# Kernel tuning notes

Measured on AMD Instinct MI355X. Metric: run time of the kernel, lower is better.

Reference implementation:

```python
import jax, jax.numpy as jnp
import numpy as np

NUM_LABELS = 1000
HIDDEN = 512
BATCH = 65536
NOISE_STD = 0.1
L_STAB, L_CENTER, L_SEP, L_BRIER = 1.0, 0.1, 0.01, 1.0


def setup_inputs() -> dict:
    key = jax.random.key(0)
    k1, k2, k3, k4, k5 = jax.random.split(key, 5)
    cls_rep = jax.random.normal(k1, (BATCH, HIDDEN), dtype=jnp.float32)
    logits = jax.random.normal(k2, (BATCH, NUM_LABELS), dtype=jnp.float32)
    labels = jax.random.randint(k3, (BATCH,), 0, NUM_LABELS)
    W = jax.random.normal(k4, (HIDDEN, NUM_LABELS), dtype=jnp.float32) * 0.02
    b = jnp.zeros((NUM_LABELS,), dtype=jnp.float32)
    noise = jax.random.normal(k5, (BATCH, HIDDEN), dtype=jnp.float32)
    centers = jnp.zeros((NUM_LABELS, HIDDEN), dtype=jnp.float32)
    return {"cls_rep": cls_rep, "logits": logits, "labels": labels,
            "W": W, "b": b, "noise": noise, "centers": centers}


def _compute_all(cls_rep, logits, labels, W, b, noise, centers):
    # --- update_centers (init branch, no_grad): per-class mean via segment_sum ---
    ones = jnp.ones((cls_rep.shape[0],), dtype=cls_rep.dtype)
    counts = jax.ops.segment_sum(ones, labels, num_segments=NUM_LABELS)           # [C]
    sums = jax.ops.segment_sum(cls_rep, labels, num_segments=NUM_LABELS)          # [C, H]
    present = counts > 0
    batch_means = sums / jnp.maximum(counts, 1.0)[:, None]
    new_centers = jnp.where(present[:, None], batch_means, centers)               # [C, H]
    new_centers = jax.lax.stop_gradient(new_centers)

    # --- stability: classifier(cls_rep + noise_std * eps) vs clean logits ---
    logits_noisy = (cls_rep + NOISE_STD * noise) @ W + b                          # [B, C]
    stab = jnp.mean((logits_noisy - logits) ** 2)

    # --- center loss: gather centroids, MSE ---
    center = jnp.mean((cls_rep - new_centers[labels]) ** 2)

    # --- separation: cdist + exp, minus exp(0)*num_labels ---
    sq = jnp.sum(new_centers ** 2, axis=1)                                        # [C]
    d2 = jnp.maximum(sq[:, None] + sq[None, :] - 2.0 * new_centers @ new_centers.T, 0.0)
    dist = jnp.sqrt(d2)                                                           # [C, C]
    I = jnp.eye(NUM_LABELS, dtype=dist.dtype)
    sep = jnp.sum(jnp.exp(-dist + I)) - jnp.float32(NUM_LABELS)

    # --- brier: softmax vs one-hot ---
    probs = jax.nn.softmax(logits, axis=-1)
    one_hot = jax.nn.one_hot(labels, NUM_LABELS, dtype=logits.dtype)
    brier = jnp.mean(jnp.sum((probs - one_hot) ** 2, axis=1))

    total = L_STAB * stab + L_CENTER * center + L_SEP * sep + L_BRIER * brier
    return jnp.stack([total, stab, center, sep, brier])


def reference(cls_rep, logits, labels, W, b, noise, centers):
    return _compute_all(cls_rep, logits, labels, W, b, noise, centers)
```

## Files before the change

kernel.cpp:

```cpp
#include <hip/hip_runtime.h>

#define BATCH 65536
#define HID   512
#define NCLS  1000
#define NCLSP 1024

typedef long i64;
typedef float f32x4 __attribute__((ext_vector_type(4)));
typedef unsigned short u16;
typedef unsigned int u32;
typedef unsigned char u8;

__device__ __forceinline__ u16 f2bf(float f) {
  u32 u = __float_as_uint(f);
  u += 0x7fffu + ((u >> 16) & 1u);
  return (u16)(u >> 16);
}

__device__ __forceinline__ u32 pk4(float a, float b, float c, float d) {
  u32 r = 0;
  r = (u32)__builtin_amdgcn_cvt_pk_fp8_f32(a, b, (int)r, false);
  r = (u32)__builtin_amdgcn_cvt_pk_fp8_f32(c, d, (int)r, true);
  return r;
}

#define WS_END 2899968
#define WS_BIG 36454400

__global__ void k_hist(const int* __restrict__ labels, int* __restrict__ counts) {
  const int i = blockIdx.x * blockDim.x + threadIdx.x;
  if (i < BATCH) atomicAdd(counts + labels[i], 1);
}

__global__ void k_scan(const int* __restrict__ counts, int* __restrict__ offsets) {
  __shared__ int tmp[1024];
  const int t = threadIdx.x;
  const int v = counts[t];
  tmp[t] = v;
  __syncthreads();
  for (int d = 1; d < 1024; d <<= 1) {
    int u = (t >= d) ? tmp[t - d] : 0;
    __syncthreads();
    tmp[t] += u;
    __syncthreads();
  }
  offsets[t] = tmp[t] - v;
}

__global__ void k_scatter(const int* __restrict__ labels, int* __restrict__ offsets,
                          int* __restrict__ order) {
  const int i = blockIdx.x * blockDim.x + threadIdx.x;
  if (i < BATCH) {
    const int pos = atomicAdd(offsets + labels[i], 1);
    order[pos] = i;
  }
}

__global__ void k_segsum(const float* __restrict__ cls, const int* __restrict__ order,
                         const int* __restrict__ offsets, const int* __restrict__ counts,
                         const float* __restrict__ cen_in, float* __restrict__ cen,
                         float* __restrict__ sq, double* __restrict__ accum) {
  __shared__ float red[8];
  __shared__ float redc[8];
  const int c = blockIdx.x;
  const int t = threadIdx.x;
  const int cnt = counts[c];
  const int end = offsets[c];
  const int start = end - cnt;
  float v;
  if (cnt > 0) {
    float s0 = 0.f, s1 = 0.f, s2 = 0.f, s3 = 0.f;
    int i = start;
    for (; i + 4 <= end; i += 4) {
      const int r0 = order[i], r1 = order[i + 1], r2 = order[i + 2], r3 = order[i + 3];
      s0 += cls[(size_t)r0 * HID + t];
      s1 += cls[(size_t)r1 * HID + t];
      s2 += cls[(size_t)r2 * HID + t];
      s3 += cls[(size_t)r3 * HID + t];
    }
    for (; i < end; ++i) s0 += cls[(size_t)order[i] * HID + t];
    v = ((s0 + s1) + (s2 + s3)) / (float)cnt;
  } else {
    v = (c < NCLS) ? cen_in[(size_t)c * HID + t] : 0.f;
  }
  cen[(size_t)c * HID + t] = v;

  float cp = 0.f;
  for (int i = start; i < end; ++i) {
    float x = cls[(size_t)order[i] * HID + t] - v;
    cp += x * x;
  }

  float p = v * v;
  #pragma unroll
  for (int s = 32; s; s >>= 1) { p += __shfl_xor(p, s); cp += __shfl_xor(cp, s); }
  if ((t & 63) == 0) { red[t >> 6] = p; redc[t >> 6] = cp; }
  __syncthreads();
  if (t == 0) {
    float acc = 0.f, accc = 0.f;
    #pragma unroll
    for (int i = 0; i < 8; ++i) { acc += red[i]; accc += redc[i]; }
    sq[c] = acc;
    atomicAdd(accum + 1, (double)accc);
  }
}

__global__ void k_wconv(const float* __restrict__ W, u32* __restrict__ wb) {
  const int j = blockIdx.x * blockDim.x + threadIdx.x;
  const int kc = j >> 13, col = (j >> 3) & 1023, kg = (j >> 1) & 3, i0 = (j & 1) * 4;
  const int k = kc * 32 + kg * 8 + i0;
  float w0 = 0.f, w1 = 0.f, w2 = 0.f, w3 = 0.f;
  if (col < NCLS) {
    w0 = W[(size_t)(k + 0) * NCLS + col] * 16.f;
    w1 = W[(size_t)(k + 1) * NCLS + col] * 16.f;
    w2 = W[(size_t)(k + 2) * NCLS + col] * 16.f;
    w3 = W[(size_t)(k + 3) * NCLS + col] * 16.f;
  }
  wb[j] = pk4(w0, w1, w2, w3);
}

__global__ void k_sep(const float* __restrict__ cen, const float* __restrict__ sq,
                      double* __restrict__ accum) {
  __shared__ float As[16][64];
  __shared__ float Bs[16][64];
  __shared__ float red[4];
  const int bi = blockIdx.x >> 4, bj = blockIdx.x & 15;
  const int tx = threadIdx.x & 15, ty = threadIdx.x >> 4;
  const int lrow = threadIdx.x & 63, lkq = threadIdx.x >> 6;
  float acc[4][4] = {};
  for (int k0 = 0; k0 < HID; k0 += 16) {
    __syncthreads();
    float4 a = *(const float4*)(cen + (size_t)(bi * 64 + lrow) * HID + k0 + lkq * 4);
    float4 b = *(const float4*)(cen + (size_t)(bj * 64 + lrow) * HID + k0 + lkq * 4);
    As[lkq*4+0][lrow] = a.x; As[lkq*4+1][lrow] = a.y; As[lkq*4+2][lrow] = a.z; As[lkq*4+3][lrow] = a.w;
    Bs[lkq*4+0][lrow] = b.x; Bs[lkq*4+1][lrow] = b.y; Bs[lkq*4+2][lrow] = b.z; Bs[lkq*4+3][lrow] = b.w;
    __syncthreads();
    #pragma unroll
    for (int k = 0; k < 16; ++k) {
      float4 av = *(const float4*)&As[k][ty * 4];
      float4 bv = *(const float4*)&Bs[k][tx * 4];
      float ar[4] = {av.x, av.y, av.z, av.w};
      float br[4] = {bv.x, bv.y, bv.z, bv.w};
      #pragma unroll
      for (int r = 0; r < 4; ++r)
        #pragma unroll
        for (int s = 0; s < 4; ++s)
          acc[r][s] = fmaf(ar[r], br[s], acc[r][s]);
    }
  }
  float part = 0.f;
  #pragma unroll
  for (int r = 0; r < 4; ++r) {
    const int i = bi * 64 + ty * 4 + r;
    #pragma unroll
    for (int s = 0; s < 4; ++s) {
      const int j = bj * 64 + tx * 4 + s;
      if (i < NCLS && j < NCLS) {
        float d2 = fmaxf(sq[i] + sq[j] - 2.f * acc[r][s], 0.f);
        float dist = sqrtf(d2);
        part += __expf((i == j ? 1.f : 0.f) - dist);
      }
    }
  }
  #pragma unroll
  for (int s = 32; s; s >>= 1) part += __shfl_xor(part, s);
  if ((threadIdx.x & 63) == 0) red[threadIdx.x >> 6] = part;
  __syncthreads();
  if (threadIdx.x == 0)
    atomicAdd(accum + 2, (double)(red[0] + red[1] + red[2] + red[3]));
}

__global__ void k_prep(const float* __restrict__ cls, const float* __restrict__ noise,
                       u8* __restrict__ panel) {
  const int nth = gridDim.x * blockDim.x;
  for (int c = blockIdx.x * blockDim.x + threadIdx.x; c < BATCH * 64; c += nth) {
    const int row = c >> 6;
    const int g = (c & 63) * 8;
    const int sw = ((row & 7) << 3) | (((row >> 3) & 1) << 6);
    const int k = g ^ sw;
    const float4* cp = (const float4*)(cls   + (size_t)row * HID + k);
    const float4* np = (const float4*)(noise + (size_t)row * HID + k);
    float4 a0 = cp[0], a1 = cp[1];
    float4 n0 = np[0], n1 = np[1];
    uint2 p;
    p.x = pk4(fmaf(0.1f, n0.x, a0.x), fmaf(0.1f, n0.y, a0.y),
              fmaf(0.1f, n0.z, a0.z), fmaf(0.1f, n0.w, a0.w));
    p.y = pk4(fmaf(0.1f, n1.x, a1.x), fmaf(0.1f, n1.y, a1.y),
              fmaf(0.1f, n1.z, a1.z), fmaf(0.1f, n1.w, a1.w));
    *(uint2*)&panel[(size_t)row * 512 + g] = p;
  }
}

__global__ __launch_bounds__(512, 4)
void k_gemm(const u8* __restrict__ panel, const float* __restrict__ logits,
            const int* __restrict__ labels, const float* __restrict__ bias,
            const u8* __restrict__ wb, double* __restrict__ accum) {
  __shared__ u16 lds[32 * 1024];
  u8* lds8 = (u8*)lds;
  const int lane = threadIdx.x & 63;
  const int w = threadIdx.x >> 6;
  const int row0 = blockIdx.x * 32;
  const int l15 = lane & 15, lkg = lane >> 4;

  {
    const u8* src = panel + (size_t)blockIdx.x * 16384;
    #pragma unroll
    for (int r = 0; r < 2; ++r) {
      const int seg = r * 8 + w;
      const u8* g = src + seg * 1024 + lane * 16;
      u8* l = lds8 + seg * 1024;
      __builtin_amdgcn_global_load_lds((const __attribute__((address_space(1))) void*)g,
                                       (__attribute__((address_space(3))) void*)l,
                                       16, 0, 0);
    }
  }
  __syncthreads();

  f32x4 acc[2][8] = {};
  const int swr = ((l15 & 7) << 3) | ((l15 >> 3) << 6);
  for (int kc = 0; kc < 16; ++kc) {
    i64 af0 = *(const i64*)&lds8[(l15)      * 512 + ((kc * 32 + lkg * 8) ^ swr)];
    i64 af1 = *(const i64*)&lds8[(16 + l15) * 512 + ((kc * 32 + lkg * 8) ^ swr)];
    const u8* bb = wb + (size_t)kc * 32768 + (w * 128 + l15) * 32 + lkg * 8;
    #pragma unroll
    for (int ct = 0; ct < 8; ++ct) {
      i64 bf = *(const i64*)(bb + ct * 512);
      acc[0][ct] = __builtin_amdgcn_mfma_f32_16x16x32_fp8_fp8(af0, bf, acc[0][ct], 0, 0, 0);
      acc[1][ct] = __builtin_amdgcn_mfma_f32_16x16x32_fp8_fp8(af1, bf, acc[1][ct], 0, 0, 0);
    }
  }

  __syncthreads();
  char* ldsb = (char*)lds;
  #pragma unroll
  for (int ct = 0; ct < 8; ++ct) {
    const int col = w * 128 + ct * 16 + l15;
    if (col < NCLS) {
      const float bc = bias[col];
      #pragma unroll
      for (int rt = 0; rt < 2; ++rt) {
        #pragma unroll
        for (int r = 0; r < 4; ++r) {
          const int rowloc = rt * 16 + lkg * 4 + r;
          const int byte = rowloc * 2048 + ((col * 2) ^ ((rowloc & 12) << 3));
          *(u16*)(ldsb + byte) = f2bf(fmaf(acc[rt][ct][r], 0.0625f, bc));
        }
      }
    }
  }
  __syncthreads();

  float spart = 0.f, bpart = 0.f;
  for (int j = 0; j < 4; ++j) {
    const int rowloc = w * 4 + j;
    const int row = row0 + rowloc;
    const int swz = (rowloc & 12) << 3;
    const char* lnrow = ldsb + rowloc * 2048;
    const float4* lr = (const float4*)(logits + (size_t)row * NCLS);
    const int lab2 = labels[row];
    float S = 0.f, S2 = 0.f, el = 0.f;
    #pragma unroll
    for (int it = 0; it < 4; ++it) {
      const int f = it * 64 + lane;
      if (f < 250) {
        float4 lg = lr[f];
        const u32* lp = (const u32*)(lnrow + ((f * 8) ^ swz));
        u32 w0 = lp[0], w1 = lp[1];
        float n0 = __uint_as_float(w0 << 16);
        float n1 = __uint_as_float(w0 & 0xffff0000u);
        float n2 = __uint_as_float(w1 << 16);
        float n3 = __uint_as_float(w1 & 0xffff0000u);
        float d0 = n0 - lg.x, d1 = n1 - lg.y, d2 = n2 - lg.z, d3 = n3 - lg.w;
        spart += d0 * d0 + d1 * d1 + d2 * d2 + d3 * d3;
        float e0 = __expf(lg.x), e1 = __expf(lg.y), e2 = __expf(lg.z), e3 = __expf(lg.w);
        S += e0 + e1 + e2 + e3;
        S2 += e0 * e0 + e1 * e1 + e2 * e2 + e3 * e3;
        const int c0 = f * 4;
        if (c0     == lab2) el = e0;
        if (c0 + 1 == lab2) el = e1;
        if (c0 + 2 == lab2) el = e2;
        if (c0 + 3 == lab2) el = e3;
      }
    }
    #pragma unroll
    for (int s = 32; s; s >>= 1) { S += __shfl_xor(S, s); S2 += __shfl_xor(S2, s); el += __shfl_xor(el, s); }
    bpart += S2 / (S * S) - 2.f * el / S + 1.f;
  }
  #pragma unroll
  for (int s = 32; s; s >>= 1) { spart += __shfl_xor(spart, s); bpart += __shfl_xor(bpart, s); }

  __syncthreads();
  float* redf = (float*)lds;
  if (lane == 0) { redf[w] = spart; redf[8 + w] = bpart; }
  __syncthreads();
  if (threadIdx.x == 0) {
    float st = 0.f, br = 0.f;
    #pragma unroll
    for (int i = 0; i < 8; ++i) { st += redf[i]; br += redf[8 + i]; }
    atomicAdd(accum + 0, (double)st);
    atomicAdd(accum + 3, (double)br);
  }
}

__global__ __launch_bounds__(512, 4)
void k_stab_fb(const float* __restrict__ cls, const float* __restrict__ noise,
               const float* __restrict__ logits, const int* __restrict__ labels,
               const float* __restrict__ bias, const u8* __restrict__ wb,
               double* __restrict__ accum) {
  __shared__ u16 lds[32 * 1024];
  u8* lds8 = (u8*)lds;
  const int lane = threadIdx.x & 63;
  const int w = threadIdx.x >> 6;
  const int row0 = blockIdx.x * 32;
  const int l15 = lane & 15, lkg = lane >> 4;
  {
    const int row_loc = threadIdx.x >> 4;
    const int k0 = (threadIdx.x & 15) * 32;
    const int sw = ((row_loc & 7) << 3) | (((row_loc >> 3) & 1) << 6);
    const float* cp = cls   + (size_t)(row0 + row_loc) * HID;
    const float* np = noise + (size_t)(row0 + row_loc) * HID;
    #pragma unroll
    for (int q = 0; q < 4; ++q) {
      const int g = k0 + q * 8;
      const int k = g ^ sw;
      float4 a0 = *(const float4*)(cp + k), a1 = *(const float4*)(cp + k + 4);
      float4 n0 = *(const float4*)(np + k), n1 = *(const float4*)(np + k + 4);
      uint2 p;
      p.x = pk4(fmaf(0.1f, n0.x, a0.x), fmaf(0.1f, n0.y, a0.y),
                fmaf(0.1f, n0.z, a0.z), fmaf(0.1f, n0.w, a0.w));
      p.y = pk4(fmaf(0.1f, n1.x, a1.x), fmaf(0.1f, n1.y, a1.y),
                fmaf(0.1f, n1.z, a1.z), fmaf(0.1f, n1.w, a1.w));
      *(uint2*)&lds8[row_loc * 512 + g] = p;
    }
  }
  __syncthreads();
  f32x4 acc[2][8] = {};
  const int swr = ((l15 & 7) << 3) | ((l15 >> 3) << 6);
  for (int kc = 0; kc < 16; ++kc) {
    i64 af0 = *(const i64*)&lds8[(l15)      * 512 + ((kc * 32 + lkg * 8) ^ swr)];
    i64 af1 = *(const i64*)&lds8[(16 + l15) * 512 + ((kc * 32 + lkg * 8) ^ swr)];
    const u8* bb = wb + (size_t)kc * 32768 + (w * 128 + l15) * 32 + lkg * 8;
    #pragma unroll
    for (int ct = 0; ct < 8; ++ct) {
      i64 bf = *(const i64*)(bb + ct * 512);
      acc[0][ct] = __builtin_amdgcn_mfma_f32_16x16x32_fp8_fp8(af0, bf, acc[0][ct], 0, 0, 0);
      acc[1][ct] = __builtin_amdgcn_mfma_f32_16x16x32_fp8_fp8(af1, bf, acc[1][ct], 0, 0, 0);
    }
  }
  __syncthreads();
  char* ldsb = (char*)lds;
  #pragma unroll
  for (int ct = 0; ct < 8; ++ct) {
    const int col = w * 128 + ct * 16 + l15;
    if (col < NCLS) {
      const float bc = bias[col];
      #pragma unroll
      for (int rt = 0; rt < 2; ++rt) {
        #pragma unroll
        for (int r = 0; r < 4; ++r) {
          const int rowloc = rt * 16 + lkg * 4 + r;
          const int byte = rowloc * 2048 + ((col * 2) ^ ((rowloc & 12) << 3));
          *(u16*)(ldsb + byte) = f2bf(fmaf(acc[rt][ct][r], 0.0625f, bc));
        }
      }
    }
  }
  __syncthreads();
  float spart = 0.f, bpart = 0.f;
  for (int j = 0; j < 4; ++j) {
    const int rowloc = w * 4 + j;
    const int row = row0 + rowloc;
    const int swz = (rowloc & 12) << 3;
    const char* lnrow = ldsb + rowloc * 2048;
    const float4* lr = (const float4*)(logits + (size_t)row * NCLS);
    const int lab2 = labels[row];
    float S = 0.f, S2 = 0.f, el = 0.f;
    #pragma unroll
    for (int it = 0; it < 4; ++it) {
      const int f = it * 64 + lane;
      if (f < 250) {
        float4 lg = lr[f];
        const u32* lp = (const u32*)(lnrow + ((f * 8) ^ swz));
        u32 w0 = lp[0], w1 = lp[1];
        float n0 = __uint_as_float(w0 << 16);
        float n1 = __uint_as_float(w0 & 0xffff0000u);
        float n2 = __uint_as_float(w1 << 16);
        float n3 = __uint_as_float(w1 & 0xffff0000u);
        float d0 = n0 - lg.x, d1 = n1 - lg.y, d2 = n2 - lg.z, d3 = n3 - lg.w;
        spart += d0 * d0 + d1 * d1 + d2 * d2 + d3 * d3;
        float e0 = __expf(lg.x), e1 = __expf(lg.y), e2 = __expf(lg.z), e3 = __expf(lg.w);
        S += e0 + e1 + e2 + e3;
        S2 += e0 * e0 + e1 * e1 + e2 * e2 + e3 * e3;
        const int c0 = f * 4;
        if (c0     == lab2) el = e0;
        if (c0 + 1 == lab2) el = e1;
        if (c0 + 2 == lab2) el = e2;
        if (c0 + 3 == lab2) el = e3;
      }
    }
    #pragma unroll
    for (int s = 32; s; s >>= 1) { S += __shfl_xor(S, s); S2 += __shfl_xor(S2, s); el += __shfl_xor(el, s); }
    bpart += S2 / (S * S) - 2.f * el / S + 1.f;
  }
  #pragma unroll
  for (int s = 32; s; s >>= 1) { spart += __shfl_xor(spart, s); bpart += __shfl_xor(bpart, s); }
  __syncthreads();
  float* redf = (float*)lds;
  if (lane == 0) { redf[w] = spart; redf[8 + w] = bpart; }
  __syncthreads();
  if (threadIdx.x == 0) {
    float st = 0.f, br = 0.f;
    #pragma unroll
    for (int i = 0; i < 8; ++i) { st += redf[i]; br += redf[8 + i]; }
    atomicAdd(accum + 0, (double)st);
    atomicAdd(accum + 3, (double)br);
  }
}

__global__ void k_final(const double* __restrict__ accum, float* __restrict__ out) {
  if (threadIdx.x == 0) {
    double stab   = accum[0] / ((double)BATCH * (double)NCLS);
    double center = accum[1] / ((double)BATCH * (double)HID);
    double sep    = accum[2] - (double)NCLS;
    double brier  = accum[3] / (double)BATCH;
    double total  = 1.0 * stab + 0.1 * center + 0.01 * sep + 1.0 * brier;
    out[0] = (float)total;
    out[1] = (float)stab;
    out[2] = (float)center;
    out[3] = (float)sep;
    out[4] = (float)brier;
  }
}

extern "C" void kernel_launch(void* const* d_in, const int* in_sizes, int n_in,
                              void* d_out, int out_size, void* d_ws, size_t ws_size,
                              hipStream_t stream) {
  const float* cls    = (const float*)d_in[0];
  const float* logits = (const float*)d_in[1];
  const int*   labels = (const int*)d_in[2];
  const float* W      = (const float*)d_in[3];
  const float* bias   = (const float*)d_in[4];
  const float* noise  = (const float*)d_in[5];
  const float* cen_in = (const float*)d_in[6];
  float* out = (float*)d_out;
  char* ws = (char*)d_ws;
  if (ws_size < (size_t)WS_END) return;

  int*    counts  = (int*)(ws + 0);
  double* accum   = (double*)(ws + 4096);
  float*  sq      = (float*)(ws + 8192);
  int*    offsets = (int*)(ws + 12288);
  int*    order   = (int*)(ws + 16384);
  float*  cen     = (float*)(ws + 278528);
  u8*     wb8     = (u8*)(ws + 2375680);
  u8*     panel8  = (u8*)(ws + 2899968);

  hipMemsetAsync(ws, 0, 4160, stream);
  hipLaunchKernelGGL(k_hist,    dim3(256),  dim3(256), 0, stream, labels, counts);
  hipLaunchKernelGGL(k_wconv,   dim3(512),  dim3(256), 0, stream, W, (u32*)wb8);
  hipLaunchKernelGGL(k_scan,    dim3(1),    dim3(1024),0, stream, counts, offsets);
  hipLaunchKernelGGL(k_scatter, dim3(256),  dim3(256), 0, stream, labels, offsets, order);
  hipLaunchKernelGGL(k_segsum,  dim3(1024), dim3(512), 0, stream, cls, order, offsets, counts, cen_in, cen, sq, accum);
  hipLaunchKernelGGL(k_sep,     dim3(256),  dim3(256), 0, stream, cen, sq, accum);
  if (ws_size >= (size_t)WS_BIG) {
    hipLaunchKernelGGL(k_prep,  dim3(2048), dim3(256), 0, stream, cls, noise, panel8);
    hipLaunchKernelGGL(k_gemm,  dim3(2048), dim3(512), 0, stream, panel8, logits, labels, bias, wb8, accum);
  } else {
    hipLaunchKernelGGL(k_stab_fb, dim3(2048), dim3(512), 0, stream, cls, noise, logits, labels, bias, wb8, accum);
  }
  hipLaunchKernelGGL(k_final,   dim3(1),    dim3(64),  0, stream, accum, out);
}
```

Before: 311.9 us.

## Fuse segsum variance pass, widen gemm block to 16 waves with fp8 noisy-logit tile

The segment-sum kernel now accumulates sum and sum of squares in one pass and derives the center loss as sumsq minus cnt*mean², dropping the second gather over cls rows. The main gemm kernel moves to 1024-thread blocks, each wave covering 64 columns, which reduces per-wave accumulators and keeps the separate LDS tiles small. Noisy logits are staged in LDS as fp8 instead of bf16, halving that tile's footprint and so making the larger block feasible. The risks are lower precision in both the stability term and the variance formula, which can cancel catastrophically.

```diff
diff --git a/kernel.cpp b/kernel.cpp
--- a/kernel.cpp
+++ b/kernel.cpp
@@ -7,6 +7,7 @@
 
 typedef long i64;
 typedef float f32x4 __attribute__((ext_vector_type(4)));
+typedef float f32x2 __attribute__((ext_vector_type(2)));
 typedef unsigned short u16;
 typedef unsigned int u32;
 typedef unsigned char u8;
@@ -22,6 +23,9 @@
   r = (u32)__builtin_amdgcn_cvt_pk_fp8_f32(a, b, (int)r, false);
   r = (u32)__builtin_amdgcn_cvt_pk_fp8_f32(c, d, (int)r, true);
   return r;
+}
+__device__ __forceinline__ u8 pk1(float a) {
+  return (u8)(__builtin_amdgcn_cvt_pk_fp8_f32(a, 0.f, 0, false) & 0xff);
 }
 
 #define WS_END 2899968
@@ -67,29 +71,33 @@
   const int cnt = counts[c];
   const int end = offsets[c];
   const int start = end - cnt;
-  float v;
+  float v, cp;
   if (cnt > 0) {
     float s0 = 0.f, s1 = 0.f, s2 = 0.f, s3 = 0.f;
+    float q0 = 0.f, q1 = 0.f, q2 = 0.f, q3 = 0.f;
     int i = start;
     for (; i + 4 <= end; i += 4) {
       const int r0 = order[i], r1 = order[i + 1], r2 = order[i + 2], r3 = order[i + 3];
-      s0 += cls[(size_t)r0 * HID + t];
-      s1 += cls[(size_t)r1 * HID + t];
-      s2 += cls[(size_t)r2 * HID + t];
-      s3 += cls[(size_t)r3 * HID + t];
-    }
-    for (; i < end; ++i) s0 += cls[(size_t)order[i] * HID + t];
+      float x0 = cls[(size_t)r0 * HID + t];
+      float x1 = cls[(size_t)r1 * HID + t];
+      float x2 = cls[(size_t)r2 * HID + t];
+      float x3 = cls[(size_t)r3 * HID + t];
+      s0 += x0; q0 = fmaf(x0, x0, q0);
+      s1 += x1; q1 = fmaf(x1, x1, q1);
+      s2 += x2; q2 = fmaf(x2, x2, q2);
+      s3 += x3; q3 = fmaf(x3, x3, q3);
+    }
+    for (; i < end; ++i) {
+      float x = cls[(size_t)order[i] * HID + t];
+      s0 += x; q0 = fmaf(x, x, q0);
+    }
     v = ((s0 + s1) + (s2 + s3)) / (float)cnt;
+    cp = ((q0 + q1) + (q2 + q3)) - (float)cnt * v * v;
   } else {
     v = (c < NCLS) ? cen_in[(size_t)c * HID + t] : 0.f;
+    cp = 0.f;
   }
   cen[(size_t)c * HID + t] = v;
-
-  float cp = 0.f;
-  for (int i = start; i < end; ++i) {
-    float x = cls[(size_t)order[i] * HID + t] - v;
-    cp += x * x;
-  }
 
   float p = v * v;
   #pragma unroll
@@ -191,31 +199,139 @@
   }
 }
 
-__global__ __launch_bounds__(512, 4)
+__global__ __launch_bounds__(1024, 8)
 void k_gemm(const u8* __restrict__ panel, const float* __restrict__ logits,
             const int* __restrict__ labels, const float* __restrict__ bias,
             const u8* __restrict__ wb, double* __restrict__ accum) {
+  __shared__ u8 Apan[32 * 512];
+  __shared__ u8 lntile[32 * 1024];
+  __shared__ float redf[32];
+  const int lane = threadIdx.x & 63;
+  const int w = threadIdx.x >> 6;
+  const int row0 = blockIdx.x * 32;
+  const int l15 = lane & 15, lkg = lane >> 4;
+
+  {
+    const u8* g = panel + (size_t)blockIdx.x * 16384 + w * 1024 + lane * 16;
+    u8* l = Apan + w * 1024;
+    __builtin_amdgcn_global_load_lds((const __attribute__((address_space(1))) void*)g,
+                                     (__attribute__((address_space(3))) void*)l,
+                                     16, 0, 0);
+  }
+  __syncthreads();
+
+  f32x4 acc[2][4] = {};
+  const int swr = ((l15 & 7) << 3) | ((l15 >> 3) << 6);
+  for (int kc = 0; kc < 16; ++kc) {
+    i64 af0 = *(const i64*)&Apan[(l15)      * 512 + ((kc * 32 + lkg * 8) ^ swr)];
+    i64 af1 = *(const i64*)&Apan[(16 + l15) * 512 + ((kc * 32 + lkg * 8) ^ swr)];
+    const u8* bb = wb + (size_t)kc * 32768 + (w * 64 + l15) * 32 + lkg * 8;
+    #pragma unroll
+    for (int ct = 0; ct < 4; ++ct) {
+      i64 bf = *(const i64*)(bb + ct * 512);
+      acc[0][ct] = __builtin_amdgcn_mfma_f32_16x16x32_fp8_fp8(af0, bf, acc[0][ct], 0, 0, 0);
+      acc[1][ct] = __builtin_amdgcn_mfma_f32_16x16x32_fp8_fp8(af1, bf, acc[1][ct], 0, 0, 0);
+    }
+  }
+
+  #pragma unroll
+  for (int ct = 0; ct < 4; ++ct) {
+    const int col = w * 64 + ct * 16 + l15;
+    if (col < NCLS) {
+      const float bc = bias[col];
+      #pragma unroll
+      for (int rt = 0; rt < 2; ++rt) {
+        #pragma unroll
+        for (int r = 0; r < 4; ++r) {
+          const int rowloc = rt * 16 + lkg * 4 + r;
+          lntile[rowloc * 1024 + (col ^ ((rowloc & 12) << 2))] =
+              pk1(fmaf(acc[rt][ct][r], 0.0625f, bc));
+        }
+      }
+    }
+  }
+  __syncthreads();
+
+  float spart = 0.f, bpart = 0.f;
+  #pragma unroll
+  for (int j = 0; j < 2; ++j) {
+    const int rowloc = w * 2 + j;
+    const int row = row0 + rowloc;
+    const int swz = (rowloc & 12) << 2;
+    const u8* lnrow = lntile + rowloc * 1024;
+    const float4* lr = (const float4*)(logits + (size_t)row * NCLS);
+    const int lab2 = labels[row];
+    float S = 0.f, S2 = 0.f, el = 0.f;
+    #pragma unroll
+    for (int it = 0; it < 4; ++it) {
+      const int f = it * 64 + lane;
+      if (f < 250) {
+        float4 lg = lr[f];
+        u32 v = *(const u32*)(lnrow + ((f * 4) ^ swz));
+        f32x2 lo = __builtin_amdgcn_cvt_pk_f32_fp8((int)v, false);
+        f32x2 hi = __builtin_amdgcn_cvt_pk_f32_fp8((int)v, true);
+        float d0 = lo[0] - lg.x, d1 = lo[1] - lg.y, d2 = hi[0] - lg.z, d3 = hi[1] - lg.w;
+        spart += d0 * d0 + d1 * d1 + d2 * d2 + d3 * d3;
+        float e0 = __expf(lg.x), e1 = __expf(lg.y), e2 = __expf(lg.z), e3 = __expf(lg.w);
+        S += e0 + e1 + e2 + e3;
+        S2 += e0 * e0 + e1 * e1 + e2 * e2 + e3 * e3;
+        const int c0 = f * 4;
+        if (c0     == lab2) el = e0;
+        if (c0 + 1 == lab2) el = e1;
+        if (c0 + 2 == lab2) el = e2;
+        if (c0 + 3 == lab2) el = e3;
+      }
+    }
+    #pragma unroll
+    for (int s = 32; s; s >>= 1) { S += __shfl_xor(S, s); S2 += __shfl_xor(S2, s); el += __shfl_xor(el, s); }
+    bpart += S2 / (S * S) - 2.f * el / S + 1.f;
+  }
+  #pragma unroll
+  for (int s = 32; s; s >>= 1) { spart += __shfl_xor(spart, s); bpart += __shfl_xor(bpart, s); }
+
+  if (lane == 0) { redf[w] = spart; redf[16 + w] = bpart; }
+  __syncthreads();
+  if (threadIdx.x == 0) {
+    float st = 0.f, br = 0.f;
+    #pragma unroll
+    for (int i = 0; i < 16; ++i) { st += redf[i]; br += redf[16 + i]; }
+    atomicAdd(accum + 0, (double)st);
+    atomicAdd(accum + 3, (double)br);
+  }
+}
+
+__global__ __launch_bounds__(512, 4)
+void k_stab_fb(const float* __restrict__ cls, const float* __restrict__ noise,
+               const float* __restrict__ logits, const int* __restrict__ labels,
+               const float* __restrict__ bias, const u8* __restrict__ wb,
+               double* __restrict__ accum) {
   __shared__ u16 lds[32 * 1024];
   u8* lds8 = (u8*)lds;
   const int lane = threadIdx.x & 63;
   const int w = threadIdx.x >> 6;
   const int row0 = blockIdx.x * 32;
   const int l15 = lane & 15, lkg = lane >> 4;
-
   {
-    const u8* src = panel + (size_t)blockIdx.x * 16384;
-    #pragma unroll
-    for (int r = 0; r < 2; ++r) {
-      const int seg = r * 8 + w;
-      const u8* g = src + seg * 1024 + lane * 16;
-      u8* l = lds8 + seg * 1024;
-      __builtin_amdgcn_global_load_lds((const __attribute__((address_space(1))) void*)g,
-                                       (__attribute__((address_space(3))) void*)l,
-                                       16, 0, 0);
-    }
-  }
-  __syncthreads();
-
+    const int row_loc = threadIdx.x >> 4;
+    const int k0 = (threadIdx.x & 15) * 32;
+    const int sw = ((row_loc & 7) << 3) | (((row_loc >> 3) & 1) << 6);
+    const float* cp = cls   + (size_t)(row0 + row_loc) * HID;
+    const float* np = noise + (size_t)(row0 + row_loc) * HID;
+    #pragma unroll
+    for (int q = 0; q < 4; ++q) {
+      const int g = k0 + q * 8;
+      const int k = g ^ sw;
+      float4 a0 = *(const float4*)(cp + k), a1 = *(const float4*)(cp + k + 4);
+      float4 n0 = *(const float4*)(np + k), n1 = *(const float4*)(np + k + 4);
+      uint2 p;
+      p.x = pk4(fmaf(0.1f, n0.x, a0.x), fmaf(0.1f, n0.y, a0.y),
+                fmaf(0.1f, n0.z, a0.z), fmaf(0.1f, n0.w, a0.w));
+      p.y = pk4(fmaf(0.1f, n1.x, a1.x), fmaf(0.1f, n1.y, a1.y),
+                fmaf(0.1f, n1.z, a1.z), fmaf(0.1f, n1.w, a1.w));
+      *(uint2*)&lds8[row_loc * 512 + g] = p;
+    }
+  }
+  __syncthreads();
   f32x4 acc[2][8] = {};
   const int swr = ((l15 & 7) << 3) | ((l15 >> 3) << 6);
   for (int kc = 0; kc < 16; ++kc) {
@@ -229,7 +345,6 @@
       acc[1][ct] = __builtin_amdgcn_mfma_f32_16x16x32_fp8_fp8(af1, bf, acc[1][ct], 0, 0, 0);
     }
   }
-
   __syncthreads();
   char* ldsb = (char*)lds;
   #pragma unroll
@@ -249,7 +364,6 @@
     }
   }
   __syncthreads();
-
   float spart = 0.f, bpart = 0.f;
   for (int j = 0; j < 4; ++j) {
     const int rowloc = w * 4 + j;
@@ -288,122 +402,6 @@
   }
   #pragma unroll
   for (int s = 32; s; s >>= 1) { spart += __shfl_xor(spart, s); bpart += __shfl_xor(bpart, s); }
-
-  __syncthreads();
-  float* redf = (float*)lds;
-  if (lane == 0) { redf[w] = spart; redf[8 + w] = bpart; }
-  __syncthreads();
-  if (threadIdx.x == 0) {
-    float st = 0.f, br = 0.f;
-    #pragma unroll
-    for (int i = 0; i < 8; ++i) { st += redf[i]; br += redf[8 + i]; }
-    atomicAdd(accum + 0, (double)st);
-    atomicAdd(accum + 3, (double)br);
-  }
-}
-
-__global__ __launch_bounds__(512, 4)
-void k_stab_fb(const float* __restrict__ cls, const float* __restrict__ noise,
-               const float* __restrict__ logits, const int* __restrict__ labels,
-               const float* __restrict__ bias, const u8* __restrict__ wb,
-               double* __restrict__ accum) {
-  __shared__ u16 lds[32 * 1024];
-  u8* lds8 = (u8*)lds;
-  const int lane = threadIdx.x & 63;
-  const int w = threadIdx.x >> 6;
-  const int row0 = blockIdx.x * 32;
-  const int l15 = lane & 15, lkg = lane >> 4;
-  {
-    const int row_loc = threadIdx.x >> 4;
-    const int k0 = (threadIdx.x & 15) * 32;
-    const int sw = ((row_loc & 7) << 3) | (((row_loc >> 3) & 1) << 6);
-    const float* cp = cls   + (size_t)(row0 + row_loc) * HID;
-    const float* np = noise + (size_t)(row0 + row_loc) * HID;
-    #pragma unroll
-    for (int q = 0; q < 4; ++q) {
-      const int g = k0 + q * 8;
-      const int k = g ^ sw;
-      float4 a0 = *(const float4*)(cp + k), a1 = *(const float4*)(cp + k + 4);
-      float4 n0 = *(const float4*)(np + k), n1 = *(const float4*)(np + k + 4);
-      uint2 p;
-      p.x = pk4(fmaf(0.1f, n0.x, a0.x), fmaf(0.1f, n0.y, a0.y),
-                fmaf(0.1f, n0.z, a0.z), fmaf(0.1f, n0.w, a0.w));
-      p.y = pk4(fmaf(0.1f, n1.x, a1.x), fmaf(0.1f, n1.y, a1.y),
-                fmaf(0.1f, n1.z, a1.z), fmaf(0.1f, n1.w, a1.w));
-      *(uint2*)&lds8[row_loc * 512 + g] = p;
-    }
-  }
-  __syncthreads();
-  f32x4 acc[2][8] = {};
-  const int swr = ((l15 & 7) << 3) | ((l15 >> 3) << 6);
-  for (int kc = 0; kc < 16; ++kc) {
-    i64 af0 = *(const i64*)&lds8[(l15)      * 512 + ((kc * 32 + lkg * 8) ^ swr)];
-    i64 af1 = *(const i64*)&lds8[(16 + l15) * 512 + ((kc * 32 + lkg * 8) ^ swr)];
-    const u8* bb = wb + (size_t)kc * 32768 + (w * 128 + l15) * 32 + lkg * 8;
-    #pragma unroll
-    for (int ct = 0; ct < 8; ++ct) {
-      i64 bf = *(const i64*)(bb + ct * 512);
-      acc[0][ct] = __builtin_amdgcn_mfma_f32_16x16x32_fp8_fp8(af0, bf, acc[0][ct], 0, 0, 0);
-      acc[1][ct] = __builtin_amdgcn_mfma_f32_16x16x32_fp8_fp8(af1, bf, acc[1][ct], 0, 0, 0);
-    }
-  }
-  __syncthreads();
-  char* ldsb = (char*)lds;
-  #pragma unroll
-  for (int ct = 0; ct < 8; ++ct) {
-    const int col = w * 128 + ct * 16 + l15;
-    if (col < NCLS) {
-      const float bc = bias[col];
-      #pragma unroll
-      for (int rt = 0; rt < 2; ++rt) {
-        #pragma unroll
-        for (int r = 0; r < 4; ++r) {
-          const int rowloc = rt * 16 + lkg * 4 + r;
-          const int byte = rowloc * 2048 + ((col * 2) ^ ((rowloc & 12) << 3));
-          *(u16*)(ldsb + byte) = f2bf(fmaf(acc[rt][ct][r], 0.0625f, bc));
-        }
-      }
-    }
-  }
-  __syncthreads();
-  float spart = 0.f, bpart = 0.f;
-  for (int j = 0; j < 4; ++j) {
-    const int rowloc = w * 4 + j;
-    const int row = row0 + rowloc;
-    const int swz = (rowloc & 12) << 3;
-    const char* lnrow = ldsb + rowloc * 2048;
-    const float4* lr = (const float4*)(logits + (size_t)row * NCLS);
-    const int lab2 = labels[row];
-    float S = 0.f, S2 = 0.f, el = 0.f;
-    #pragma unroll
-    for (int it = 0; it < 4; ++it) {
-      const int f = it * 64 + lane;
-      if (f < 250) {
-        float4 lg = lr[f];
-        const u32* lp = (const u32*)(lnrow + ((f * 8) ^ swz));
-        u32 w0 = lp[0], w1 = lp[1];
-        float n0 = __uint_as_float(w0 << 16);
-        float n1 = __uint_as_float(w0 & 0xffff0000u);
-        float n2 = __uint_as_float(w1 << 16);
-        float n3 = __uint_as_float(w1 & 0xffff0000u);
-        float d0 = n0 - lg.x, d1 = n1 - lg.y, d2 = n2 - lg.z, d3 = n3 - lg.w;
-        spart += d0 * d0 + d1 * d1 + d2 * d2 + d3 * d3;
-        float e0 = __expf(lg.x), e1 = __expf(lg.y), e2 = __expf(lg.z), e3 = __expf(lg.w);
-        S += e0 + e1 + e2 + e3;
-        S2 += e0 * e0 + e1 * e1 + e2 * e2 + e3 * e3;
-        const int c0 = f * 4;
-        if (c0     == lab2) el = e0;
-        if (c0 + 1 == lab2) el = e1;
-        if (c0 + 2 == lab2) el = e2;
-        if (c0 + 3 == lab2) el = e3;
-      }
-    }
-    #pragma unroll
-    for (int s = 32; s; s >>= 1) { S += __shfl_xor(S, s); S2 += __shfl_xor(S2, s); el += __shfl_xor(el, s); }
-    bpart += S2 / (S * S) - 2.f * el / S + 1.f;
-  }
-  #pragma unroll
-  for (int s = 32; s; s >>= 1) { spart += __shfl_xor(spart, s); bpart += __shfl_xor(bpart, s); }
   __syncthreads();
   float* redf = (float*)lds;
   if (lane == 0) { redf[w] = spart; redf[8 + w] = bpart; }
@@ -464,7 +462,7 @@
   hipLaunchKernelGGL(k_sep,     dim3(256),  dim3(256), 0, stream, cen, sq, accum);
   if (ws_size >= (size_t)WS_BIG) {
     hipLaunchKernelGGL(k_prep,  dim3(2048), dim3(256), 0, stream, cls, noise, panel8);
-    hipLaunchKernelGGL(k_gemm,  dim3(2048), dim3(512), 0, stream, panel8, logits, labels, bias, wb8, accum);
+    hipLaunchKernelGGL(k_gemm,  dim3(2048), dim3(1024), 0, stream, panel8, logits, labels, bias, wb8, accum);
   } else {
     hipLaunchKernelGGL(k_stab_fb, dim3(2048), dim3(512), 0, stream, cls, noise, logits, labels, bias, wb8, accum);
   }
```

Result: faster. 289.7 us (-7.1%).
